# Performance work log

Hardware: AMD Instinct MI355X
Metric: run time of the kernel (lower is better)

## Reference

```python
import jax, jax.numpy as jnp
import numpy as np

IN_CH, OUT_CH, K, UP = 512, 256, 3, 2
WSCALE = float(1.0 / np.sqrt(K * K * IN_CH))  # use_wscale gain / sqrt(fan_in), lr_mul=1
ACT_GAIN = float(np.sqrt(2.0))                # lrelu def_gain
CLAMP = 256.0                                  # conv_clamp * runtime_gain(=1)
FIR_PAD = 1                                    # px0+pxt = px1+pxt = 1 (derived in forward)

def _fir_filter():
    # upfirdn2d.setup_filter([1,3,3,1]): outer product then normalize to sum 1
    f1 = jnp.array([1.0, 3.0, 3.0, 1.0], jnp.float32)
    f2 = jnp.outer(f1, f1)
    return f2 / jnp.sum(f2)  # (4,4), sums to 1

def setup_inputs() -> dict:
    key = jax.random.key(0)
    k1, k2 = jax.random.split(key)
    return {
        "x": jax.random.normal(k1, (16, IN_CH, 64, 64), jnp.float32),
        "weight": jax.random.normal(k2, (OUT_CH, IN_CH, K, K), jnp.float32),
        "bias": jnp.zeros((OUT_CH,), jnp.float32),
    }

def _forward(x, weight, bias):
    w = weight * WSCALE  # runtime weight scaling
    # torch conv_transpose2d(x, w.transpose(0,1), stride=UP, padding=0)
    # == lhs-dilated correlation with spatially flipped kernel, pad K-1 each side
    k = w[:, :, ::-1, ::-1]
    y = jax.lax.conv_general_dilated(
        x, k, window_strides=(1, 1),
        padding=((K - 1, K - 1), (K - 1, K - 1)),
        lhs_dilation=(UP, UP),
        dimension_numbers=('NCHW', 'OIHW', 'NCHW'))  # (N, OUT_CH, 129, 129)
    # upfirdn2d(up=1, padding=(1,1,1,1), gain=UP**2):
    # pad, then depthwise conv with flipped filter scaled by gain**(ndim/2)=UP*UP
    f = _fir_filter() * (UP * UP)
    y = jnp.pad(y, ((0, 0), (0, 0), (FIR_PAD, FIR_PAD), (FIR_PAD, FIR_PAD)))
    fk = jnp.broadcast_to(f[::-1, ::-1][None, None], (OUT_CH, 1, 4, 4))
    y = jax.lax.conv_general_dilated(
        y, fk, (1, 1), 'VALID',
        feature_group_count=OUT_CH,
        dimension_numbers=('NCHW', 'OIHW', 'NCHW'))  # (N, OUT_CH, 128, 128)
    # bias_act: bias add, leaky_relu(0.2), gain sqrt(2), clamp +-256
    y = y + bias[None, :, None, None]
    y = jnp.where(y >= 0, y, 0.2 * y) * ACT_GAIN
    return jnp.clip(y, -CLAMP, CLAMP)

def reference(x, weight, bias):
    return _forward(x, weight, bias)
```

## Files before the change

kernel.cpp:

```cpp
#include <hip/hip_runtime.h>
#include <hip/hip_bf16.h>

#define NIMG 16
#define IN_CH 512
#define OUT_CH 256
#define HIN 64
#define HOUT 128
#define HP 66

#define WSCALE 0.014731391f
#define ACT_GAIN 1.41421356237f
#define CLAMP_V 256.0f

typedef __attribute__((ext_vector_type(8))) short bf16x8;
typedef __attribute__((ext_vector_type(4))) float f32x4;
typedef __attribute__((ext_vector_type(16))) float f32x16;

__device__ __constant__ float c_G[2][3][3] = {
    {{0.00f, 0.25f, 0.75f}, {0.75f, 0.75f, 0.25f}, {0.25f, 0.00f, 0.00f}},
    {{0.00f, 0.00f, 0.25f}, {0.25f, 0.75f, 0.75f}, {0.75f, 0.25f, 0.00f}}
};

#define XBF_BYTES ((size_t)NIMG * HP * HP * IN_CH * 2)
#define EBF_BYTES ((size_t)9 * 1024 * IN_CH * 2)
#define WS_NEED (XBF_BYTES + EBF_BYTES)

__global__ __launch_bounds__(256) void xpose_kernel(const float* __restrict__ x,
                                                    __hip_bfloat16* __restrict__ xbf) {
    const int n = blockIdx.z;
    const int hp = blockIdx.y;
    const int c0 = blockIdx.x << 6;
    const int tid = threadIdx.x;
    const size_t obase = ((size_t)n * HP + hp) * HP;

    if (hp == 0 || hp == HP - 1) {
        for (int idx = tid; idx < HP * 64; idx += 256) {
            int wp = idx >> 6, c = idx & 63;
            xbf[(obase + wp) * IN_CH + c0 + c] = __float2bfloat16(0.f);
        }
        return;
    }
    __shared__ float tile[64][65];
    {
        int cc = tid >> 6, w = tid & 63;
        for (int cb = 0; cb < 64; cb += 4)
            tile[cb + cc][w] =
                x[(((size_t)n * IN_CH + c0 + cb + cc) * HIN + (hp - 1)) * HIN + w];
    }
    __syncthreads();
    {
        int c = tid & 63, wg = tid >> 6;
        for (int wb = 0; wb < 64; wb += 4) {
            int w2 = wb + wg;
            xbf[(obase + (w2 + 1)) * IN_CH + c0 + c] = __float2bfloat16(tile[c][w2]);
        }
        if (tid < 128) {
            int which = tid >> 6, c2 = tid & 63;
            xbf[(obase + (which ? (HP - 1) : 0)) * IN_CH + c0 + c2] = __float2bfloat16(0.f);
        }
    }
}

__global__ __launch_bounds__(256) void build_ebf_kernel(const float* __restrict__ w,
                                                        __hip_bfloat16* __restrict__ ebf) {
    int gid = blockIdx.x * 256 + threadIdx.x;
    if (gid >= OUT_CH * IN_CH) return;
    int oc = gid >> 9, c = gid & 511;
    float wm[3][3];
    const float* wp = w + (size_t)gid * 9;
#pragma unroll
    for (int a = 0; a < 3; ++a)
#pragma unroll
        for (int b = 0; b < 3; ++b) wm[a][b] = wp[a * 3 + b] * WSCALE;
#pragma unroll
    for (int i = 0; i < 3; ++i)
#pragma unroll
        for (int j = 0; j < 3; ++j)
#pragma unroll
            for (int pu = 0; pu < 2; ++pu)
#pragma unroll
                for (int pv = 0; pv < 2; ++pv) {
                    float s = 0.f;
#pragma unroll
                    for (int a = 0; a < 3; ++a)
#pragma unroll
                        for (int b = 0; b < 3; ++b)
                            s += wm[a][b] * c_G[pu][i][a] * c_G[pv][j][b];
                    ebf[((size_t)(i * 3 + j) * 1024 + oc * 4 + pu * 2 + pv) * IN_CH + c] =
                        __float2bfloat16(s);
                }
}

#define MFMA8(AF, BF, MH)                                                                   \
    do {                                                                                    \
        acc[(MH)*4+0] = __builtin_amdgcn_mfma_f32_32x32x16_bf16((AF)[0], (BF)[0], acc[(MH)*4+0], 0, 0, 0); \
        acc[(MH)*4+1] = __builtin_amdgcn_mfma_f32_32x32x16_bf16((AF)[0], (BF)[2], acc[(MH)*4+1], 0, 0, 0); \
        acc[(MH)*4+2] = __builtin_amdgcn_mfma_f32_32x32x16_bf16((AF)[2], (BF)[0], acc[(MH)*4+2], 0, 0, 0); \
        acc[(MH)*4+3] = __builtin_amdgcn_mfma_f32_32x32x16_bf16((AF)[2], (BF)[2], acc[(MH)*4+3], 0, 0, 0); \
        acc[(MH)*4+0] = __builtin_amdgcn_mfma_f32_32x32x16_bf16((AF)[1], (BF)[1], acc[(MH)*4+0], 0, 0, 0); \
        acc[(MH)*4+1] = __builtin_amdgcn_mfma_f32_32x32x16_bf16((AF)[1], (BF)[3], acc[(MH)*4+1], 0, 0, 0); \
        acc[(MH)*4+2] = __builtin_amdgcn_mfma_f32_32x32x16_bf16((AF)[3], (BF)[1], acc[(MH)*4+2], 0, 0, 0); \
        acc[(MH)*4+3] = __builtin_amdgcn_mfma_f32_32x32x16_bf16((AF)[3], (BF)[3], acc[(MH)*4+3], 0, 0, 0); \
    } while (0)

#define CJA_B 540672
#define CJB_B 131072
#define DAK1(PAR) (((((PAR) ^ 1) << 2) | 1) << 14)
#define DBK1(PAR) (((((PAR) ^ 1) << 2) | 3) << 14)
#define DAK0(PAR) ((((PAR) << 2) | 0) << 14)
#define DBK0(PAR) ((((PAR) << 2) | 2) << 14)

#define GLL(SRC, DSTOFF)                                                          \
    __builtin_amdgcn_global_load_lds(                                             \
        (const __attribute__((address_space(1))) unsigned int*)(SRC),             \
        (__attribute__((address_space(3))) unsigned int*)(ldsW + (DSTOFF)), 16, 0, 0)

#define TILE_ITER(PAR, TT, SP01, SP23, VMS, LGK3, LAST)                           \
    {                                                                             \
        const int a0 = (PAR) ? aOffO0 : aOffE0;                                   \
        const int a1 = (PAR) ? aOffO1 : aOffE1;                                   \
        const int c0 = (PAR) ? bOffO0 : bOffE0;                                   \
        const int c1 = (PAR) ? bOffO1 : bOffE1;                                   \
        \
        afO[0] = *(const bf16x8*)&lds[a0 + 4096];                                 \
        afO[1] = *(const bf16x8*)&lds[a1 + 4096];                                 \
        afO[2] = *(const bf16x8*)&lds[a0 + 4096 + 2048];                          \
        afO[3] = *(const bf16x8*)&lds[a1 + 4096 + 2048];                          \
        if (SP01) { GLL(xbc + sA1 + voffA, DAK1(PAR));                            \
                    GLL(xbc + sA1 + voffA + CJA_B, DAK1(PAR) + 8192); }           \
        sA1 += ((TT) == 22 || (TT) == 46) ? 64640 : 128;                          \
        asm volatile("s_waitcnt lgkmcnt(4)" ::: "memory");                        \
        __builtin_amdgcn_sched_barrier(0);                                        \
        __builtin_amdgcn_s_setprio(1);                                            \
        MFMA8(afE, b0, 0);                                                        \
        __builtin_amdgcn_s_setprio(0);                                            \
        asm volatile("s_waitcnt " VMS ::: "memory");                              \
        __builtin_amdgcn_s_barrier();                                             \
        __builtin_amdgcn_sched_barrier(0);                                        \
          \
        afE[0] = *(const bf16x8*)&lds[a0 + 16384];                                \
        afE[1] = *(const bf16x8*)&lds[a1 + 16384];                                \
        afE[2] = *(const bf16x8*)&lds[a0 + 16384 + 2048];                         \
        afE[3] = *(const bf16x8*)&lds[a1 + 16384 + 2048];                         \
        b1[0] = *(const bf16x8*)&lds[c0 + 16384];                                 \
        b1[1] = *(const bf16x8*)&lds[c1 + 16384];                                 \
        b1[2] = *(const bf16x8*)&lds[c0 + 16384 + 2048];                          \
        b1[3] = *(const bf16x8*)&lds[c1 + 16384 + 2048];                          \
        if (SP01) { GLL(ebc + sB1 + voffB, DBK1(PAR));                            \
                    GLL(ebc + sB1 + voffB + CJB_B, DBK1(PAR) + 8192); }           \
        sB1 += (((TT) & 7) == 6) ? 1047680 : 128;                                 \
        asm volatile("s_waitcnt lgkmcnt(8)" ::: "memory");                        \
        __builtin_amdgcn_sched_barrier(0);                                        \
        __builtin_amdgcn_s_setprio(1);                                            \
        MFMA8(afO, b0, 1);                                                        \
        __builtin_amdgcn_s_setprio(0);                                            \
        __builtin_amdgcn_s_barrier();                                             \
        __builtin_amdgcn_sched_barrier(0);                                        \
        \
        afO[0] = *(const bf16x8*)&lds[a0 + 16384 + 4096];                         \
        afO[1] = *(const bf16x8*)&lds[a1 + 16384 + 4096];                         \
        afO[2] = *(const bf16x8*)&lds[a0 + 16384 + 4096 + 2048];                  \
        afO[3] = *(const bf16x8*)&lds[a1 + 16384 + 4096 + 2048];                  \
        if (SP23) { GLL(xbc + sA0 + voffA, DAK0(PAR));                            \
                    GLL(xbc + sA0 + voffA + CJA_B, DAK0(PAR) + 8192); }           \
        sA0 += ((TT) == 21 || (TT) == 45) ? 64640 : 128;                          \
        asm volatile("s_waitcnt lgkmcnt(4)" ::: "memory");                        \
        __builtin_amdgcn_sched_barrier(0);                                        \
        __builtin_amdgcn_s_setprio(1);                                            \
        MFMA8(afE, b1, 0);                                                        \
        __builtin_amdgcn_s_setprio(0);                                            \
        asm volatile("s_waitcnt " VMS ::: "memory");                              \
        __builtin_amdgcn_s_barrier();                                             \
        __builtin_amdgcn_sched_barrier(0);                                        \
           \
        if (!(LAST)) {                                                            \
            const int na0 = (PAR) ? aOffE0 : aOffO0;                              \
            const int na1 = (PAR) ? aOffE1 : aOffO1;                              \
            const int nc0 = (PAR) ? bOffE0 : bOffO0;                              \
            const int nc1 = (PAR) ? bOffE1 : bOffO1;                              \
            afE[0] = *(const bf16x8*)&lds[na0];                                   \
            afE[1] = *(const bf16x8*)&lds[na1];                                   \
            afE[2] = *(const bf16x8*)&lds[na0 + 2048];                            \
            afE[3] = *(const bf16x8*)&lds[na1 + 2048];                            \
            b0[0] = *(const bf16x8*)&lds[nc0];                                    \
            b0[1] = *(const bf16x8*)&lds[nc1];                                    \
            b0[2] = *(const bf16x8*)&lds[nc0 + 2048];                             \
            b0[3] = *(const bf16x8*)&lds[nc1 + 2048];                             \
        }                                                                         \
        if (SP23) { GLL(ebc + sB0 + voffB, DBK0(PAR));                            \
                    GLL(ebc + sB0 + voffB + CJB_B, DBK0(PAR) + 8192); }           \
        sB0 += (((TT) & 7) == 5) ? 1047680 : 128;                                 \
        asm volatile("s_waitcnt " LGK3 ::: "memory");                             \
        __builtin_amdgcn_sched_barrier(0);                                        \
        __builtin_amdgcn_s_setprio(1);                                            \
        MFMA8(afO, b1, 1);                                                        \
        __builtin_amdgcn_s_setprio(0);                                            \
        __builtin_amdgcn_s_barrier();                                             \
        __builtin_amdgcn_sched_barrier(0);                                        \
    }

__global__ __launch_bounds__(512, 2) void mfma_conv8_kernel(
    const __hip_bfloat16* __restrict__ xbf, const __hip_bfloat16* __restrict__ ebf,
    const float* __restrict__ bias, float* __restrict__ out) {
    __shared__ __align__(16) char lds[131072];

    const int tid = threadIdx.x;
    const int lane = tid & 63;
    const int wid = tid >> 6;
    const int wy = wid >> 2;
    const int wx = wid & 3;

    const int bid = blockIdx.x;
    const int wkid = ((bid & 7) << 7) + (bid >> 3);
    const int mtile = wkid >> 2;
    const int ntile = wkid & 3;
    const int n = mtile >> 4;
    const int sub = mtile & 15;
    const int qh0 = (sub >> 2) << 4;
    const int qw0 = (sub & 3) << 4;
    const int n0 = ntile << 8;

    const int qc_s = lane >> 2;
    const int src_slot = (((lane & 3) ^ (((lane >> 4) & 1) + 2 * ((lane >> 3) & 1))) << 3);

    f32x16 acc[8];
#pragma unroll
    for (int j = 0; j < 8; ++j) acc[j] = (f32x16)(0.f);

    char* ldsW = lds + (wid << 10);
    const char* xbc = (const char*)xbf;
    const char* ebc = (const char*)ebf;

    auto stage = [&](int s) {
        const int tt2 = s >> 2;
        const int part = s & 3;
        const int mat = part & 1;
        const int kh = part >> 1;
        const int tap = tt2 >> 3;
        const int chan = ((tt2 & 7) << 6) + (kh << 5) + src_slot;
        char* dst = lds + ((((tt2 & 1) << 2) | (mat << 1) | kh) << 14) + (wid << 10);
        if (mat == 0) {
            const int fi = (tap * 171) >> 9;
            const int fj = tap - fi * 3;
            const int wp = qw0 + fj + qc_s;
#pragma unroll
            for (int c = 0; c < 2; ++c) {
                const int hp = qh0 + fi + (c << 3) + wid;
                const __hip_bfloat16* src =
                    xbf + (((size_t)n * HP + hp) * HP + wp) * IN_CH + chan;
                __builtin_amdgcn_global_load_lds(
                    (const __attribute__((address_space(1))) unsigned int*)src,
                    (__attribute__((address_space(3))) unsigned int*)(dst + (c << 13)),
                    16, 0, 0);
            }
        } else {
#pragma unroll
            for (int c = 0; c < 2; ++c) {
                const int r = (c << 7) + (wid << 4) + qc_s;
                const __hip_bfloat16* src =
                    ebf + ((size_t)tap * 1024 + n0 + r) * IN_CH + chan;
                __builtin_amdgcn_global_load_lds(
                    (const __attribute__((address_space(1))) unsigned int*)src,
                    (__attribute__((address_space(3))) unsigned int*)(dst + (c << 13)),
                    16, 0, 0);
            }
        }
    };

    const int key = ((lane >> 2) & 1) + 2 * ((lane >> 1) & 1);
    const int sl = lane >> 5;
    const int arow = ((wy << 7) + (lane & 31)) * 64;
    const int aOffE0 = arow + ((sl ^ key) << 4);
    const int aOffE1 = arow + (((sl | 2) ^ key) << 4);
    const int aOffO0 = aOffE0 + 65536;
    const int aOffO1 = aOffE1 + 65536;
    const int brow = 32768 + ((wx << 6) + (lane & 31)) * 64;
    const int bOffE0 = brow + ((sl ^ key) << 4);
    const int bOffE1 = brow + (((sl | 2) ^ key) << 4);
    const int bOffO0 = bOffE0 + 65536;
    const int bOffO1 = bOffE1 + 65536;

    const int voffA = ((((n * HP + qh0 + wid) * HP + qw0 + qc_s) * IN_CH) + src_slot) * 2;
    const int voffB = (((n0 + (wid << 4) + qc_s) * IN_CH) + src_slot) * 2;
    int sA1 = 192, sA0 = 256, sB1 = 192, sB0 = 256;

#pragma unroll
    for (int s = 0; s < 6; ++s) stage(s);
    asm volatile("s_waitcnt vmcnt(8)" ::: "memory");
    __builtin_amdgcn_s_barrier();
    __builtin_amdgcn_sched_barrier(0);

    bf16x8 afE[4], afO[4], b0[4], b1[4];
    afE[0] = *(const bf16x8*)&lds[aOffE0];
    afE[1] = *(const bf16x8*)&lds[aOffE1];
    afE[2] = *(const bf16x8*)&lds[aOffE0 + 2048];
    afE[3] = *(const bf16x8*)&lds[aOffE1 + 2048];
    b0[0] = *(const bf16x8*)&lds[bOffE0];
    b0[1] = *(const bf16x8*)&lds[bOffE1];
    b0[2] = *(const bf16x8*)&lds[bOffE0 + 2048];
    b0[3] = *(const bf16x8*)&lds[bOffE1 + 2048];

#pragma unroll 1
    for (int tt = 0; tt < 68; tt += 2) {
        TILE_ITER(0, tt, 1, 1, "vmcnt(6)", "lgkmcnt(8)", 0);
        TILE_ITER(1, tt + 1, 1, 1, "vmcnt(6)", "lgkmcnt(8)", 0);
    }
    TILE_ITER(0, 68, 1, 1, "vmcnt(6)", "lgkmcnt(8)", 0);
    TILE_ITER(1, 69, 1, 1, "vmcnt(0)", "lgkmcnt(8)", 0);
    TILE_ITER(0, 70, 1, 0, "vmcnt(0)", "lgkmcnt(8)", 0);
    TILE_ITER(1, 71, 0, 0, "vmcnt(0)", "lgkmcnt(0)", 1);

    float bv[2];
#pragma unroll
    for (int nt = 0; nt < 2; ++nt)
        bv[nt] = bias[(n0 + (wx << 6) + (nt << 5) + (lane & 31)) >> 2];
#pragma unroll
    for (int j = 0; j < 8; ++j) {
        const int mt = j >> 1, nt = j & 1;
        const int nn = n0 + (wx << 6) + (nt << 5) + (lane & 31);
        const int oc = nn >> 2, pu = (nn >> 1) & 1, pv = nn & 1;
#pragma unroll
        for (int v = 0; v < 16; ++v) {
            const int m = (wy << 7) + (mt << 5) + (v & 3) + ((v >> 2) << 3) + (sl << 2);
            const int qr = m >> 4, qc = m & 15;
            const int hb = 2 * (qh0 + qr), wb = 2 * (qw0 + qc);
            float val = acc[j][v] + bv[nt];
            val = (val >= 0.f ? val : 0.2f * val) * ACT_GAIN;
            val = fminf(fmaxf(val, -CLAMP_V), CLAMP_V);
            out[(((size_t)n * OUT_CH + oc) * HOUT + (hb + pu)) * HOUT + (wb + pv)] = val;
        }
    }
}

__global__ void build_e_kernel(const float* __restrict__ w, float* __restrict__ e_ws) {
    int gid = blockIdx.x * blockDim.x + threadIdx.x;
    if (gid >= OUT_CH * IN_CH) return;
    float wm[3][3];
    const float* wp = w + (size_t)gid * 9;
#pragma unroll
    for (int a = 0; a < 3; ++a)
#pragma unroll
        for (int b = 0; b < 3; ++b) wm[a][b] = wp[a * 3 + b] * WSCALE;
    float* op = e_ws + (size_t)gid * 36;
#pragma unroll
    for (int i = 0; i < 3; ++i)
#pragma unroll
        for (int j = 0; j < 3; ++j)
#pragma unroll
            for (int pu = 0; pu < 2; ++pu)
#pragma unroll
                for (int pv = 0; pv < 2; ++pv) {
                    float s = 0.f;
#pragma unroll
                    for (int a = 0; a < 3; ++a)
#pragma unroll
                        for (int b = 0; b < 3; ++b)
                            s += wm[a][b] * c_G[pu][i][a] * c_G[pv][j][b];
                    op[(i * 3 + j) * 4 + pu * 2 + pv] = s;
                }
}

#define OGB 8
#define CB 8
#define QT 16
__global__ __launch_bounds__(256) void fused_conv_kernel(
    const float* __restrict__ x, const float* __restrict__ e_ws,
    const float* __restrict__ bias, float* __restrict__ out) {
    __shared__ float sX[CB][18][19];
    __shared__ float4 sE[OGB * CB * 9];
    const int tid = threadIdx.x;
    const int o2 = tid >> 7;
    const int qy = (tid >> 3) & 15;
    const int qxp = tid & 7;
    const int tileIdx = blockIdx.x;
    const int hq0 = (tileIdx >> 2) * QT;
    const int wq0 = (tileIdx & 3) * QT;
    const int o0 = blockIdx.y * OGB;
    const int n = blockIdx.z;
    float4 acc[2][4];
#pragma unroll
    for (int q = 0; q < 2; ++q)
#pragma unroll
        for (int oo = 0; oo < 4; ++oo) acc[q][oo] = make_float4(0.f, 0.f, 0.f, 0.f);
    for (int c0 = 0; c0 < IN_CH; c0 += CB) {
        for (int idx = tid; idx < CB * 18 * 18; idx += 256) {
            int cc = idx / 324;
            int rem = idx - cc * 324;
            int r = rem / 18;
            int col = rem - r * 18;
            int h = hq0 - 1 + r;
            int ww = wq0 - 1 + col;
            float v = 0.f;
            if (h >= 0 && h < HIN && ww >= 0 && ww < HIN)
                v = x[(((size_t)n * IN_CH + (c0 + cc)) * HIN + h) * HIN + ww];
            sX[cc][r][col] = v;
        }
        {
            float* sEf = (float*)sE;
            for (int idx = tid; idx < OGB * CB * 36; idx += 256) {
                int ol = idx / (CB * 36);
                int rem = idx - ol * (CB * 36);
                sEf[ol * (CB * 36) + rem] =
                    e_ws[((size_t)(o0 + ol) * IN_CH + c0) * 36 + rem];
            }
        }
        __syncthreads();
#pragma unroll 1
        for (int cc = 0; cc < CB; ++cc) {
#pragma unroll
            for (int i = 0; i < 3; ++i) {
#pragma unroll
                for (int j = 0; j < 3; ++j) {
                    float xv0 = sX[cc][qy + i][2 * qxp + j];
                    float xv1 = sX[cc][qy + i][2 * qxp + 1 + j];
#pragma unroll
                    for (int oo = 0; oo < 4; ++oo) {
                        float4 e = sE[((o2 * 4 + oo) * CB + cc) * 9 + i * 3 + j];
                        acc[0][oo].x += xv0 * e.x; acc[0][oo].y += xv0 * e.y;
                        acc[0][oo].z += xv0 * e.z; acc[0][oo].w += xv0 * e.w;
                        acc[1][oo].x += xv1 * e.x; acc[1][oo].y += xv1 * e.y;
                        acc[1][oo].z += xv1 * e.z; acc[1][oo].w += xv1 * e.w;
                    }
                }
            }
        }
        __syncthreads();
    }
#pragma unroll
    for (int q = 0; q < 2; ++q) {
        int qx = 2 * qxp + q;
        int u0 = 2 * (hq0 + qy);
        int v0 = 2 * (wq0 + qx);
#pragma unroll
        for (int oo = 0; oo < 4; ++oo) {
            int o = o0 + o2 * 4 + oo;
            float b = bias[o];
            float vals[4] = {acc[q][oo].x, acc[q][oo].y, acc[q][oo].z, acc[q][oo].w};
#pragma unroll
            for (int p = 0; p < 4; ++p) {
                int pu = p >> 1, pv = p & 1;
                float v = vals[p] + b;
                v = (v >= 0.f ? v : 0.2f * v) * ACT_GAIN;
                v = fminf(fmaxf(v, -CLAMP_V), CLAMP_V);
                out[(((size_t)n * OUT_CH + o) * HOUT + (u0 + pu)) * HOUT + (v0 + pv)] = v;
            }
        }
    }
}

extern "C" void kernel_launch(void* const* d_in, const int* in_sizes, int n_in,
                              void* d_out, int out_size, void* d_ws, size_t ws_size,
                              hipStream_t stream) {
    const float* x = (const float*)d_in[0];
    const float* w = (const float*)d_in[1];
    const float* bias = (const float*)d_in[2];
    float* out = (float*)d_out;

    if (ws_size >= WS_NEED) {
        __hip_bfloat16* xbf = (__hip_bfloat16*)d_ws;
        __hip_bfloat16* ebf = (__hip_bfloat16*)((char*)d_ws + XBF_BYTES);
        xpose_kernel<<<dim3(8, HP, NIMG), 256, 0, stream>>>(x, xbf);
        build_ebf_kernel<<<(OUT_CH * IN_CH + 255) / 256, 256, 0, stream>>>(w, ebf);
        mfma_conv8_kernel<<<dim3(1024), 512, 0, stream>>>(xbf, ebf, bias, out);
    } else {
        float* e_ws = (float*)d_ws;
        build_e_kernel<<<(OUT_CH * IN_CH + 255) / 256, 256, 0, stream>>>(w, e_ws);
        dim3 grid(16, OUT_CH / OGB, NIMG);
        fused_conv_kernel<<<grid, 256, 0, stream>>>(x, e_ws, bias, out);
    }
}
```

Measured before the change: 664.3 us.

## Reorganize LDS tile layout so each wave loads a full 16-byte slice of contiguous rows

Changes how global-to-LDS loads map lanes to rows and channel slices. Each wave now covers one 16-byte channel slice across 64 consecutive rows instead of 16 rows by four slots, and the XOR swizzle becomes a simple 64-byte flip. The MFMA fragment read offsets are recomputed to match the new layout. The aim is fewer LDS bank conflicts on fragment reads and a simpler address setup, at the cost of a different global access pattern, since each lane now fetches one 16-byte chunk per row with a 1 KB stride.

```diff
diff --git a/kernel.cpp b/kernel.cpp
--- a/kernel.cpp
+++ b/kernel.cpp
@@ -103,8 +103,8 @@
         acc[(MH)*4+3] = __builtin_amdgcn_mfma_f32_32x32x16_bf16((AF)[3], (BF)[3], acc[(MH)*4+3], 0, 0, 0); \
     } while (0)
 
-#define CJA_B 540672
-#define CJB_B 131072
+#define CDA 270336
+#define CDB 65536
 #define DAK1(PAR) (((((PAR) ^ 1) << 2) | 1) << 14)
 #define DBK1(PAR) (((((PAR) ^ 1) << 2) | 3) << 14)
 #define DAK0(PAR) ((((PAR) << 2) | 0) << 14)
@@ -117,17 +117,17 @@
 
 #define TILE_ITER(PAR, TT, SP01, SP23, VMS, LGK3, LAST)                           \
     {                                                                             \
-        const int a0 = (PAR) ? aOffO0 : aOffE0;                                   \
-        const int a1 = (PAR) ? aOffO1 : aOffE1;                                   \
-        const int c0 = (PAR) ? bOffO0 : bOffE0;                                   \
-        const int c1 = (PAR) ? bOffO1 : bOffE1;                                   \
+        const int A0 = (PAR) ? aM0O : aM0E;                                       \
+        const int A1 = (PAR) ? aM1O : aM1E;                                       \
+        const int B0 = (PAR) ? bN0O : bN0E;                                       \
+        const int B1 = (PAR) ? bN1O : bN1E;                                       \
         \
-        afO[0] = *(const bf16x8*)&lds[a0 + 4096];                                 \
-        afO[1] = *(const bf16x8*)&lds[a1 + 4096];                                 \
-        afO[2] = *(const bf16x8*)&lds[a0 + 4096 + 2048];                          \
-        afO[3] = *(const bf16x8*)&lds[a1 + 4096 + 2048];                          \
+        afO[0] = *(const bf16x8*)&lds[A0 + 1024];                                 \
+        afO[1] = *(const bf16x8*)&lds[A0 + 1024 + 8192];                          \
+        afO[2] = *(const bf16x8*)&lds[A1 + 1024];                                 \
+        afO[3] = *(const bf16x8*)&lds[A1 + 1024 + 8192];                          \
         if (SP01) { GLL(xbc + sA1 + voffA, DAK1(PAR));                            \
-                    GLL(xbc + sA1 + voffA + CJA_B, DAK1(PAR) + 8192); }           \
+                    GLL(xbc + sA1 + voffA + CDA, DAK1(PAR) + 1024); }             \
         sA1 += ((TT) == 22 || (TT) == 46) ? 64640 : 128;                          \
         asm volatile("s_waitcnt lgkmcnt(4)" ::: "memory");                        \
         __builtin_amdgcn_sched_barrier(0);                                        \
@@ -138,16 +138,16 @@
         __builtin_amdgcn_s_barrier();                                             \
         __builtin_amdgcn_sched_barrier(0);                                        \
           \
-        afE[0] = *(const bf16x8*)&lds[a0 + 16384];                                \
-        afE[1] = *(const bf16x8*)&lds[a1 + 16384];                                \
-        afE[2] = *(const bf16x8*)&lds[a0 + 16384 + 2048];                         \
-        afE[3] = *(const bf16x8*)&lds[a1 + 16384 + 2048];                         \
-        b1[0] = *(const bf16x8*)&lds[c0 + 16384];                                 \
-        b1[1] = *(const bf16x8*)&lds[c1 + 16384];                                 \
-        b1[2] = *(const bf16x8*)&lds[c0 + 16384 + 2048];                          \
-        b1[3] = *(const bf16x8*)&lds[c1 + 16384 + 2048];                          \
+        afE[0] = *(const bf16x8*)&lds[A0 + 16384];                                \
+        afE[1] = *(const bf16x8*)&lds[A0 + 16384 + 8192];                         \
+        afE[2] = *(const bf16x8*)&lds[A1 + 16384];                                \
+        afE[3] = *(const bf16x8*)&lds[A1 + 16384 + 8192];                         \
+        b1[0] = *(const bf16x8*)&lds[B0 + 16384];                                 \
+        b1[1] = *(const bf16x8*)&lds[B0 + 16384 + 8192];                          \
+        b1[2] = *(const bf16x8*)&lds[B1 + 16384];                                 \
+        b1[3] = *(const bf16x8*)&lds[B1 + 16384 + 8192];                          \
         if (SP01) { GLL(ebc + sB1 + voffB, DBK1(PAR));                            \
-                    GLL(ebc + sB1 + voffB + CJB_B, DBK1(PAR) + 8192); }           \
+                    GLL(ebc + sB1 + voffB + CDB, DBK1(PAR) + 1024); }             \
         sB1 += (((TT) & 7) == 6) ? 1047680 : 128;                                 \
         asm volatile("s_waitcnt lgkmcnt(8)" ::: "memory");                        \
         __builtin_amdgcn_sched_barrier(0);                                        \
@@ -157,12 +157,12 @@
         __builtin_amdgcn_s_barrier();                                             \
         __builtin_amdgcn_sched_barrier(0);                                        \
         \
-        afO[0] = *(const bf16x8*)&lds[a0 + 16384 + 4096];                         \
-        afO[1] = *(const bf16x8*)&lds[a1 + 16384 + 4096];                         \
-        afO[2] = *(const bf16x8*)&lds[a0 + 16384 + 4096 + 2048];                  \
-        afO[3] = *(const bf16x8*)&lds[a1 + 16384 + 4096 + 2048];                  \
+        afO[0] = *(const bf16x8*)&lds[A0 + 16384 + 1024];                         \
+        afO[1] = *(const bf16x8*)&lds[A0 + 16384 + 1024 + 8192];                  \
+        afO[2] = *(const bf16x8*)&lds[A1 + 16384 + 1024];                         \
+        afO[3] = *(const bf16x8*)&lds[A1 + 16384 + 1024 + 8192];                  \
         if (SP23) { GLL(xbc + sA0 + voffA, DAK0(PAR));                            \
-                    GLL(xbc + sA0 + voffA + CJA_B, DAK0(PAR) + 8192); }           \
+                    GLL(xbc + sA0 + voffA + CDA, DAK0(PAR) + 1024); }             \
         sA0 += ((TT) == 21 || (TT) == 45) ? 64640 : 128;                          \
         asm volatile("s_waitcnt lgkmcnt(4)" ::: "memory");                        \
         __builtin_amdgcn_sched_barrier(0);                                        \
@@ -174,21 +174,21 @@
         __builtin_amdgcn_sched_barrier(0);                                        \
            \
         if (!(LAST)) {                                                            \
-            const int na0 = (PAR) ? aOffE0 : aOffO0;                              \
-            const int na1 = (PAR) ? aOffE1 : aOffO1;                              \
-            const int nc0 = (PAR) ? bOffE0 : bOffO0;                              \
-            const int nc1 = (PAR) ? bOffE1 : bOffO1;                              \
-            afE[0] = *(const bf16x8*)&lds[na0];                                   \
-            afE[1] = *(const bf16x8*)&lds[na1];                                   \
-            afE[2] = *(const bf16x8*)&lds[na0 + 2048];                            \
-            afE[3] = *(const bf16x8*)&lds[na1 + 2048];                            \
-            b0[0] = *(const bf16x8*)&lds[nc0];                                    \
-            b0[1] = *(const bf16x8*)&lds[nc1];                                    \
-            b0[2] = *(const bf16x8*)&lds[nc0 + 2048];                             \
-            b0[3] = *(const bf16x8*)&lds[nc1 + 2048];                             \
+            const int nA0 = (PAR) ? aM0E : aM0O;                                  \
+            const int nA1 = (PAR) ? aM1E : aM1O;                                  \
+            const int nB0 = (PAR) ? bN0E : bN0O;                                  \
+            const int nB1 = (PAR) ? bN1E : bN1O;                                  \
+            afE[0] = *(const bf16x8*)&lds[nA0];                                   \
+            afE[1] = *(const bf16x8*)&lds[nA0 + 8192];                            \
+            afE[2] = *(const bf16x8*)&lds[nA1];                                   \
+            afE[3] = *(const bf16x8*)&lds[nA1 + 8192];                            \
+            b0[0] = *(const bf16x8*)&lds[nB0];                                    \
+            b0[1] = *(const bf16x8*)&lds[nB0 + 8192];                             \
+            b0[2] = *(const bf16x8*)&lds[nB1];                                    \
+            b0[3] = *(const bf16x8*)&lds[nB1 + 8192];                             \
         }                                                                         \
         if (SP23) { GLL(ebc + sB0 + voffB, DBK0(PAR));                            \
-                    GLL(ebc + sB0 + voffB + CJB_B, DBK0(PAR) + 8192); }           \
+                    GLL(ebc + sB0 + voffB + CDB, DBK0(PAR) + 1024); }             \
         sB0 += (((TT) & 7) == 5) ? 1047680 : 128;                                 \
         asm volatile("s_waitcnt " LGK3 ::: "memory");                             \
         __builtin_amdgcn_sched_barrier(0);                                        \
@@ -220,68 +220,53 @@
     const int qw0 = (sub & 3) << 4;
     const int n0 = ntile << 8;
 
-    const int qc_s = lane >> 2;
-    const int src_slot = (((lane & 3) ^ (((lane >> 4) & 1) + 2 * ((lane >> 3) & 1))) << 3);
+    const int slice = wid & 3;
+    const int rowhalf = wid >> 2;
 
     f32x16 acc[8];
 #pragma unroll
     for (int j = 0; j < 8; ++j) acc[j] = (f32x16)(0.f);
 
-    char* ldsW = lds + (wid << 10);
+    char* ldsW = lds + (slice << 12) + (rowhalf << 11);
     const char* xbc = (const char*)xbf;
     const char* ebc = (const char*)ebf;
+
+    const int q = lane ^ ((lane & 32) ? 4 : 0) ^ ((slice & 1) ? 4 : 0);
+    const int voffA =
+        ((n * HP + qh0 + (rowhalf << 3) + (q >> 4)) * HP + qw0 + (q & 15)) * 1024 +
+        (slice << 4);
+    const int voffB = ((n0 + (rowhalf << 7) + q) << 10) + (slice << 4);
 
     auto stage = [&](int s) {
         const int tt2 = s >> 2;
         const int part = s & 3;
         const int mat = part & 1;
         const int kh = part >> 1;
-        const int tap = tt2 >> 3;
-        const int chan = ((tt2 & 7) << 6) + (kh << 5) + src_slot;
-        char* dst = lds + ((((tt2 & 1) << 2) | (mat << 1) | kh) << 14) + (wid << 10);
-        if (mat == 0) {
-            const int fi = (tap * 171) >> 9;
-            const int fj = tap - fi * 3;
-            const int wp = qw0 + fj + qc_s;
-#pragma unroll
-            for (int c = 0; c < 2; ++c) {
-                const int hp = qh0 + fi + (c << 3) + wid;
-                const __hip_bfloat16* src =
-                    xbf + (((size_t)n * HP + hp) * HP + wp) * IN_CH + chan;
-                __builtin_amdgcn_global_load_lds(
-                    (const __attribute__((address_space(1))) unsigned int*)src,
-                    (__attribute__((address_space(3))) unsigned int*)(dst + (c << 13)),
-                    16, 0, 0);
-            }
-        } else {
-#pragma unroll
-            for (int c = 0; c < 2; ++c) {
-                const int r = (c << 7) + (wid << 4) + qc_s;
-                const __hip_bfloat16* src =
-                    ebf + ((size_t)tap * 1024 + n0 + r) * IN_CH + chan;
-                __builtin_amdgcn_global_load_lds(
-                    (const __attribute__((address_space(1))) unsigned int*)src,
-                    (__attribute__((address_space(3))) unsigned int*)(dst + (c << 13)),
-                    16, 0, 0);
-            }
+        const int slot = (((tt2 & 1) << 2) | (mat << 1) | kh) << 14;
+        const int scal = tt2 * 128 + kh * 64;
+#pragma unroll
+        for (int c = 0; c < 2; ++c) {
+            const char* src = mat == 0 ? (xbc + voffA + scal + c * CDA)
+                                       : (ebc + voffB + scal + c * CDB);
+            __builtin_amdgcn_global_load_lds(
+                (const __attribute__((address_space(1))) unsigned int*)src,
+                (__attribute__((address_space(3))) unsigned int*)(ldsW + slot + c * 1024),
+                16, 0, 0);
         }
     };
 
-    const int key = ((lane >> 2) & 1) + 2 * ((lane >> 1) & 1);
     const int sl = lane >> 5;
-    const int arow = ((wy << 7) + (lane & 31)) * 64;
-    const int aOffE0 = arow + ((sl ^ key) << 4);
-    const int aOffE1 = arow + (((sl | 2) ^ key) << 4);
-    const int aOffO0 = aOffE0 + 65536;
-    const int aOffO1 = aOffE1 + 65536;
-    const int brow = 32768 + ((wx << 6) + (lane & 31)) * 64;
-    const int bOffE0 = brow + ((sl ^ key) << 4);
-    const int bOffE1 = brow + (((sl | 2) ^ key) << 4);
-    const int bOffO0 = bOffE0 + 65536;
-    const int bOffO1 = bOffE1 + 65536;
-
-    const int voffA = ((((n * HP + qh0 + wid) * HP + qw0 + qc_s) * IN_CH) + src_slot) * 2;
-    const int voffB = (((n0 + (wid << 4) + qc_s) * IN_CH) + src_slot) * 2;
+    const int l31 = lane & 31;
+    const int sx = sl ? 64 : 0;
+    const int aM0E = (sl << 12) + (wy << 11) + ((l31 << 4) ^ sx);
+    const int aM1E = (sl << 12) + (wy << 11) + 512 + ((l31 << 4) ^ 64 ^ sx);
+    const int aM0O = aM0E + 65536;
+    const int aM1O = aM1E + 65536;
+    const int bN0E = 32768 + (sl << 12) + (wx << 10) + ((l31 << 4) ^ sx);
+    const int bN1E = 32768 + (sl << 12) + (wx << 10) + 512 + ((l31 << 4) ^ 64 ^ sx);
+    const int bN0O = bN0E + 65536;
+    const int bN1O = bN1E + 65536;
+
     int sA1 = 192, sA0 = 256, sB1 = 192, sB0 = 256;
 
 #pragma unroll
@@ -291,14 +276,14 @@
     __builtin_amdgcn_sched_barrier(0);
 
     bf16x8 afE[4], afO[4], b0[4], b1[4];
-    afE[0] = *(const bf16x8*)&lds[aOffE0];
-    afE[1] = *(const bf16x8*)&lds[aOffE1];
-    afE[2] = *(const bf16x8*)&lds[aOffE0 + 2048];
-    afE[3] = *(const bf16x8*)&lds[aOffE1 + 2048];
-    b0[0] = *(const bf16x8*)&lds[bOffE0];
-    b0[1] = *(const bf16x8*)&lds[bOffE1];
-    b0[2] = *(const bf16x8*)&lds[bOffE0 + 2048];
-    b0[3] = *(const bf16x8*)&lds[bOffE1 + 2048];
+    afE[0] = *(const bf16x8*)&lds[aM0E];
+    afE[1] = *(const bf16x8*)&lds[aM0E + 8192];
+    afE[2] = *(const bf16x8*)&lds[aM1E];
+    afE[3] = *(const bf16x8*)&lds[aM1E + 8192];
+    b0[0] = *(const bf16x8*)&lds[bN0E];
+    b0[1] = *(const bf16x8*)&lds[bN0E + 8192];
+    b0[2] = *(const bf16x8*)&lds[bN1E];
+    b0[3] = *(const bf16x8*)&lds[bN1E + 8192];
 
 #pragma unroll 1
     for (int tt = 0; tt < 68; tt += 2) {
@@ -313,11 +298,11 @@
     float bv[2];
 #pragma unroll
     for (int nt = 0; nt < 2; ++nt)
-        bv[nt] = bias[(n0 + (wx << 6) + (nt << 5) + (lane & 31)) >> 2];
+        bv[nt] = bias[(n0 + (wx << 6) + (nt << 5) + l31) >> 2];
 #pragma unroll
     for (int j = 0; j < 8; ++j) {
         const int mt = j >> 1, nt = j & 1;
-        const int nn = n0 + (wx << 6) + (nt << 5) + (lane & 31);
+        const int nn = n0 + (wx << 6) + (nt << 5) + l31;
         const int oc = nn >> 2, pu = (nn >> 1) & 1, pv = nn & 1;
 #pragma unroll
         for (int v = 0; v < 16; ++v) {
```

New measurement: 735.3 us. 1.11x slower.
